# Kernel tuning notes

Hardware: AMD Instinct MI355X
Metric: run time of the kernel (lower is better)

The kernel has to match this reference:

```python
import jax, jax.numpy as jnp
import numpy as np

B, S, D, H, DK, CR = 4, 4096, 1024, 16, 64, 3


def setup_inputs() -> dict:
    rng = jax.random.key(0)
    ks = jax.random.split(rng, 13)
    sc = 1.0 / np.sqrt(D)
    u = lambda k, shape: jax.random.uniform(k, shape, jnp.float32, -sc, sc)
    return {
        "query": jax.random.normal(ks[0], (B, S, D), jnp.float32),
        "key": jax.random.normal(ks[1], (B, S, D), jnp.float32),
        "value": jax.random.normal(ks[2], (B, S, D), jnp.float32),
        "Wq": u(ks[3], (D, D)), "bq": u(ks[4], (D,)),
        "Wk": u(ks[5], (D, D)), "bk": u(ks[6], (D,)),
        "Wv": u(ks[7], (D, D)), "bv": u(ks[8], (D,)),
        "Wo": u(ks[9], (D, D)), "bo": u(ks[10], (D,)),
        "conv_w": u(ks[11], (D, D, CR)),  # Conv1d(D, D, kernel=CR, stride=CR)
        "conv_b": u(ks[12], (D,)),
    }


def _compress(x, w, b):
    # x: (B, L, D) -> strided conv over L -> (B, ceil-ish L/CR, D)
    y = jax.lax.conv_general_dilated(
        x.transpose(0, 2, 1), w, window_strides=(CR,), padding="VALID",
        dimension_numbers=("NCH", "OIH", "NCH"))
    return (y + b[None, :, None]).transpose(0, 2, 1)


def reference(query, key, value, Wq, bq, Wk, bk, Wv, bv, Wo, bo, conv_w, conv_b):
    # Source quirk: pad amount derived from d_model (last dim), applied to seq.
    pad = CR - D % CR  # = 2 here
    if pad < CR:
        key = jnp.pad(key, ((0, 0), (pad, 0), (0, 0)))
        value = jnp.pad(value, ((0, 0), (pad, 0), (0, 0)))
    key = _compress(key, conv_w, conv_b)
    value = _compress(value, conv_w, conv_b)

    def proj(x, W, bias):  # (B, L, D) -> (B, H, L, DK)
        return (x @ W.T + bias).reshape(x.shape[0], -1, H, DK).transpose(0, 2, 1, 3)

    q = proj(query, Wq, bq)
    k = proj(key, Wk, bk)
    v = proj(value, Wv, bv)

    scores = jnp.einsum("bhqd,bhkd->bhqk", q, k) / np.float32(np.sqrt(DK))
    attn = jax.nn.softmax(scores, axis=-1)  # dropout is identity at eval
    x = jnp.einsum("bhqk,bhkd->bhqd", attn, v)
    x = x.transpose(0, 2, 1, 3).reshape(query.shape[0], -1, H * DK)
    return x @ Wo.T + bo
```

## Files before the change

### kernel.cpp

```cpp
#include <hip/hip_runtime.h>


#define DM   1024
#define NH   16
#define DKH  64
#define BB   4
#define SQ   4096
#define LCC  1366
#define LCP  1408
#define SPAD 4098

#define QSC  0.18033688011f

typedef unsigned short u16;
using short8 = __attribute__((ext_vector_type(8))) short;
using f32x4  = __attribute__((ext_vector_type(4))) float;
using us4    = __attribute__((ext_vector_type(4))) unsigned short;
using us8    = __attribute__((ext_vector_type(8))) unsigned short;

__device__ __forceinline__ u16 f2bf(float f) {
    unsigned u = __float_as_uint(f);
    u += 0x7fffu + ((u >> 16) & 1u);
    return (u16)(u >> 16);
}

__device__ __forceinline__ void gl_lds16(const void* g, void* l) {
    __builtin_amdgcn_global_load_lds(
        (__attribute__((address_space(1))) unsigned int*)(uintptr_t)g,
        (__attribute__((address_space(3))) unsigned int*)l,
        16, 0, 0);
}

__global__ __launch_bounds__(256) void cast4_k(const float* __restrict__ in, u16* __restrict__ out,
                                               int n4, float scale) {
    int i = blockIdx.x * 256 + threadIdx.x;
    if (i >= n4) return;
    float4 v = ((const float4*)in)[i];
    us4 o;
    o[0] = f2bf(v.x * scale); o[1] = f2bf(v.y * scale);
    o[2] = f2bf(v.z * scale); o[3] = f2bf(v.w * scale);
    ((us4*)out)[i] = o;
}

__global__ __launch_bounds__(256) void cast_pad2_k(const float* __restrict__ in0, u16* __restrict__ out0,
                                                   const float* __restrict__ in1, u16* __restrict__ out1) {
    const float* in = blockIdx.z ? in1 : in0;
    u16* out        = blockIdx.z ? out1 : out0;
    int i = blockIdx.x * 256 + threadIdx.x;
    const int n4 = BB * SPAD * DM / 4;
    if (i >= n4) return;
    int e   = i * 4;
    int b   = e / (SPAD * DM);
    int rem = e - b * (SPAD * DM);
    int s   = rem >> 10;
    int d   = rem & (DM - 1);
    us4 o = {0, 0, 0, 0};
    if (s >= 2) {
        float4 v = *(const float4*)(in + (size_t)(b * SQ + (s - 2)) * DM + d);
        o[0] = f2bf(v.x); o[1] = f2bf(v.y); o[2] = f2bf(v.z); o[3] = f2bf(v.w);
    }
    ((us4*)out)[i] = o;
}

__global__ __launch_bounds__(256) void permcast_conv_k(const float* __restrict__ cw, u16* __restrict__ wc2) {
    int i = blockIdx.x * 256 + threadIdx.x;
    const int n4 = DM * DM * 3 / 4;
    if (i >= n4) return;
    int e   = i * 4;
    int o   = e / 3072;
    int rem = e - o * 3072;
    int r   = rem >> 10;
    int ii  = rem & 1023;
    us4 q;
    #pragma unroll
    for (int t = 0; t < 4; ++t) q[t] = f2bf(cw[(size_t)(o * DM + ii + t) * 3 + r]);
    ((us4*)wc2)[i] = q;
}

__global__ __launch_bounds__(256) void transpose_v_k(const u16* __restrict__ vp, u16* __restrict__ vt) {
    __shared__ u16 t[64 * 65];
    const int tid = threadIdx.x;
    const int j0 = blockIdx.x * 64;
    const int bh = blockIdx.y, b = bh >> 4, h = bh & 15;
    #pragma unroll
    for (int it = 0; it < 2; ++it) {
        int cc = tid + it * 256;
        int j = cc >> 3, d0 = (cc & 7) * 8;
        int jj = j0 + j;
        us8 v = {0, 0, 0, 0, 0, 0, 0, 0};
        if (jj < LCC) v = *(const us8*)(vp + (size_t)(b * LCC + jj) * DM + h * DKH + d0);
        #pragma unroll
        for (int q = 0; q < 8; ++q) t[(d0 + q) * 65 + j] = v[q];
    }
    __syncthreads();
    #pragma unroll
    for (int it = 0; it < 2; ++it) {
        int cc = tid + it * 256;
        int d = cc >> 3, q0 = (cc & 7) * 8;
        us8 v;
        #pragma unroll
        for (int q = 0; q < 8; ++q) {
            int cp = q0 + q;
            int ks = cp >> 5, qd = (cp >> 3) & 3, j = cp & 7;
            int k  = (ks + 2 * (j >> 2)) * 16 + qd * 4 + (j & 3);
            v[q] = t[d * 65 + k];
        }
        *(us8*)(vt + (size_t)(bh * DKH + d) * LCP + j0 + q0) = v;
    }
}

__global__ __launch_bounds__(256, 3) void gemm_mfma_k(
    const u16* __restrict__ A0, const u16* __restrict__ B0, const float* __restrict__ bias0, void* __restrict__ C0,
    const u16* __restrict__ A1, const u16* __restrict__ B1, const float* __restrict__ bias1, void* __restrict__ C1,
    int N, int K, int cf32, float bscale)
{
    const u16* A     = blockIdx.z ? A1 : A0;
    const u16* Bw    = blockIdx.z ? B1 : B0;
    const float* bias = blockIdx.z ? bias1 : bias0;
    void* C          = blockIdx.z ? C1 : C0;

    __shared__ u16 As[128 * 64];
    __shared__ u16 Bs[128 * 64];
    const int tid = threadIdx.x, wave = tid >> 6, lane = tid & 63;
    const int quad = lane >> 4, l15 = lane & 15;
    const int n0 = blockIdx.y * 128, o0 = blockIdx.x * 128;
    const int wm = (wave >> 1) * 64, wn = (wave & 1) * 64;

    f32x4 acc[4][4];
    #pragma unroll
    for (int a = 0; a < 4; ++a)
        #pragma unroll
        for (int b = 0; b < 4; ++b)
            #pragma unroll
            for (int r = 0; r < 4; ++r) acc[a][b][r] = 0.0f;

    const int srow = (lane >> 3);
    const int sc8  = (lane & 7);

    for (int kt = 0; kt < K; kt += 64) {
        #pragma unroll
        for (int i = 0; i < 4; ++i) {
            int is  = wave * 4 + i;
            int row = is * 8 + srow;
            int c   = sc8 ^ (row & 7);
            int ra  = n0 + row; if (ra > N - 1) ra = N - 1;
            gl_lds16(A  + (size_t)ra * K + kt + c * 8,          As + is * 512 + lane * 8);
            gl_lds16(Bw + (size_t)(o0 + row) * K + kt + c * 8,  Bs + is * 512 + lane * 8);
        }
        __syncthreads();
        #pragma unroll
        for (int ks = 0; ks < 2; ++ks) {
            short8 af[4], bf[4];
            #pragma unroll
            for (int mi = 0; mi < 4; ++mi) {
                int m = wm + mi * 16 + l15;
                int c = (ks * 4 + quad) ^ (m & 7);
                af[mi] = *(const short8*)(As + m * 64 + c * 8);
            }
            #pragma unroll
            for (int nj = 0; nj < 4; ++nj) {
                int n = wn + nj * 16 + l15;
                int c = (ks * 4 + quad) ^ (n & 7);
                bf[nj] = *(const short8*)(Bs + n * 64 + c * 8);
            }
            #pragma unroll
            for (int mi = 0; mi < 4; ++mi)
                #pragma unroll
                for (int nj = 0; nj < 4; ++nj)
                    acc[mi][nj] = __builtin_amdgcn_mfma_f32_16x16x32_bf16(af[mi], bf[nj], acc[mi][nj], 0, 0, 0);
        }
        __syncthreads();
    }
    #pragma unroll
    for (int mi = 0; mi < 4; ++mi) {
        #pragma unroll
        for (int r = 0; r < 4; ++r) {
            int n = n0 + wm + mi * 16 + quad * 4 + r;
            if (n < N) {
                #pragma unroll
                for (int nj = 0; nj < 4; ++nj) {
                    int o = o0 + wn + nj * 16 + l15;
                    float v = acc[mi][nj][r] + bias[o] * bscale;
                    if (cf32) ((float*)C)[(size_t)n * DM + o] = v;
                    else      ((u16*)C)[(size_t)n * DM + o] = f2bf(v);
                }
            }
        }
    }
}

__global__ __launch_bounds__(256, 3) void attn_mfma_k(
    const u16* __restrict__ qp, const u16* __restrict__ kp,
    const u16* __restrict__ vt, u16* __restrict__ xo)
{
    __shared__ u16 lds[4 * 4096];
    const int tid = threadIdx.x, wave = tid >> 6, lane = tid & 63;
    const int quad = lane >> 4, l15 = lane & 15;
    const int bh = blockIdx.y, b = bh >> 4, h = bh & 15;
    const int s0 = blockIdx.x * 128;
    const int wq = wave * 32;
    const int srow = lane >> 3, sc8 = lane & 7;

    #pragma unroll
    for (int i = 0; i < 4; ++i) {
        int is = wave * 4 + i;
        int row = is * 8 + srow;
        int c = sc8 ^ (row & 7);
        gl_lds16(qp + (size_t)(b * SQ + s0 + row) * DM + h * DKH + c * 8,
                 lds + is * 512 + lane * 8);
    }
    __syncthreads();
    short8 qfr[2][2];
    #pragma unroll
    for (int qg = 0; qg < 2; ++qg) {
        int m = wq + qg * 16 + l15;
        #pragma unroll
        for (int ks = 0; ks < 2; ++ks) {
            int c = (ks * 4 + quad) ^ (m & 7);
            qfr[qg][ks] = *(const short8*)(lds + m * 64 + c * 8);
        }
    }
    __syncthreads();

    f32x4 oacc[2][4];
    #pragma unroll
    for (int a = 0; a < 2; ++a)
        #pragma unroll
        for (int d = 0; d < 4; ++d)
            #pragma unroll
            for (int r = 0; r < 4; ++r) oacc[a][d][r] = 0.0f;
    float lsum[2] = {0.f, 0.f};

    #pragma unroll
    for (int i = 0; i < 2; ++i) {
        int is = wave * 2 + i;
        int row = is * 8 + srow;
        int c = sc8 ^ (row & 7);
        int j = row; if (j > LCC - 1) j = LCC - 1;
        gl_lds16(kp + (size_t)(b * LCC + j) * DM + h * DKH + c * 8, lds + is * 512 + lane * 8);
        gl_lds16(vt + (size_t)(bh * DKH + row) * LCP + c * 8,       lds + 4096 + is * 512 + lane * 8);
    }

    int cur = 0;
    for (int t = 0; t < 22; ++t) {
        const int j0 = t * 64;
        __syncthreads();
        if (t < 21) {
            int nj0 = j0 + 64;
            u16* base = lds + (cur ^ 1) * 8192;
            #pragma unroll
            for (int i = 0; i < 2; ++i) {
                int is = wave * 2 + i;
                int row = is * 8 + srow;
                int c = sc8 ^ (row & 7);
                int j = nj0 + row; if (j > LCC - 1) j = LCC - 1;
                gl_lds16(kp + (size_t)(b * LCC + j) * DM + h * DKH + c * 8, base + is * 512 + lane * 8);
                gl_lds16(vt + (size_t)(bh * DKH + row) * LCP + nj0 + c * 8, base + 4096 + is * 512 + lane * 8);
            }
        }
        const u16* Kb = lds + cur * 8192;
        const u16* Vb = Kb + 4096;

        f32x4 sc[2][4];
        #pragma unroll
        for (int a = 0; a < 2; ++a)
            #pragma unroll
            for (int n = 0; n < 4; ++n)
                #pragma unroll
                for (int r = 0; r < 4; ++r) sc[a][n][r] = 0.0f;
        __builtin_amdgcn_s_setprio(1);
        #pragma unroll
        for (int ks = 0; ks < 2; ++ks) {
            short8 kfr[4];
            #pragma unroll
            for (int nj = 0; nj < 4; ++nj) {
                int n = nj * 16 + l15;
                int c = (ks * 4 + quad) ^ (n & 7);
                kfr[nj] = *(const short8*)(Kb + n * 64 + c * 8);
            }
            #pragma unroll
            for (int qg = 0; qg < 2; ++qg)
                #pragma unroll
                for (int nj = 0; nj < 4; ++nj)
                    sc[qg][nj] = __builtin_amdgcn_mfma_f32_16x16x32_bf16(kfr[nj], qfr[qg][ks], sc[qg][nj], 0, 0, 0);
        }
        __builtin_amdgcn_s_setprio(0);

        const bool tail = (j0 + 64 > LCC);
        #pragma unroll
        for (int qg = 0; qg < 2; ++qg) {
            #pragma unroll
            for (int nj = 0; nj < 4; ++nj) {
                #pragma unroll
                for (int r = 0; r < 4; ++r) {
                    float p = __builtin_amdgcn_exp2f(sc[qg][nj][r]);
                    if (tail && (j0 + nj * 16 + quad * 4 + r) >= LCC) p = 0.0f;
                    sc[qg][nj][r] = p;
                    lsum[qg] += p;
                }
            }
        }
        short8 pa[2][2];
        #pragma unroll
        for (int qg = 0; qg < 2; ++qg) {
            #pragma unroll
            for (int ks = 0; ks < 2; ++ks) {
                unsigned w0, w1, w2, w3;
                asm("v_cvt_pk_bf16_f32 %0, %1, %2" : "=v"(w0) : "v"(sc[qg][ks][0]),     "v"(sc[qg][ks][1]));
                asm("v_cvt_pk_bf16_f32 %0, %1, %2" : "=v"(w1) : "v"(sc[qg][ks][2]),     "v"(sc[qg][ks][3]));
                asm("v_cvt_pk_bf16_f32 %0, %1, %2" : "=v"(w2) : "v"(sc[qg][ks + 2][0]), "v"(sc[qg][ks + 2][1]));
                asm("v_cvt_pk_bf16_f32 %0, %1, %2" : "=v"(w3) : "v"(sc[qg][ks + 2][2]), "v"(sc[qg][ks + 2][3]));
                union { unsigned u[4]; short8 s; } cv;
                cv.u[0] = w0; cv.u[1] = w1; cv.u[2] = w2; cv.u[3] = w3;
                pa[qg][ks] = cv.s;
            }
        }
        __builtin_amdgcn_s_setprio(1);
        #pragma unroll
        for (int ks = 0; ks < 2; ++ks) {
            short8 vfr[4];
            #pragma unroll
            for (int dj = 0; dj < 4; ++dj) {
                int d = dj * 16 + l15;
                int c = (ks * 4 + quad) ^ (d & 7);
                vfr[dj] = *(const short8*)(Vb + d * 64 + c * 8);
            }
            #pragma unroll
            for (int qg = 0; qg < 2; ++qg)
                #pragma unroll
                for (int dj = 0; dj < 4; ++dj)
                    oacc[qg][dj] = __builtin_amdgcn_mfma_f32_16x16x32_bf16(pa[qg][ks], vfr[dj], oacc[qg][dj], 0, 0, 0);
        }
        __builtin_amdgcn_s_setprio(0);
        cur ^= 1;
    }

    #pragma unroll
    for (int qg = 0; qg < 2; ++qg) {
        float v = lsum[qg];
        v += __shfl_xor(v, 16, 64);
        v += __shfl_xor(v, 32, 64);
        lsum[qg] = v;
    }
    #pragma unroll
    for (int qg = 0; qg < 2; ++qg) {
        #pragma unroll
        for (int r = 0; r < 4; ++r) {
            float tot = __shfl(lsum[qg], quad * 4 + r, 64);
            float inv = 1.0f / tot;
            int s = s0 + wq + qg * 16 + quad * 4 + r;
            #pragma unroll
            for (int dj = 0; dj < 4; ++dj)
                xo[(size_t)(b * SQ + s) * DM + h * DKH + dj * 16 + l15] = f2bf(oacc[qg][dj][r] * inv);
        }
    }
}

extern "C" void kernel_launch(void* const* d_in, const int* in_sizes, int n_in,
                              void* d_out, int out_size, void* d_ws, size_t ws_size,
                              hipStream_t stream)
{
    const float* query  = (const float*)d_in[0];
    const float* key    = (const float*)d_in[1];
    const float* value  = (const float*)d_in[2];
    const float* Wq     = (const float*)d_in[3];
    const float* bq     = (const float*)d_in[4];
    const float* Wk     = (const float*)d_in[5];
    const float* bk     = (const float*)d_in[6];
    const float* Wv     = (const float*)d_in[7];
    const float* bv     = (const float*)d_in[8];
    const float* Wo     = (const float*)d_in[9];
    const float* bo     = (const float*)d_in[10];
    const float* conv_w = (const float*)d_in[11];
    const float* conv_b = (const float*)d_in[12];
    float* out = (float*)d_out;

    u16* p = (u16*)d_ws;
    auto alloc = [&](size_t n) { u16* r = p; p += (n + 127) & ~(size_t)127; return r; };
    u16* qbf  = alloc((size_t)BB * SQ * DM);
    u16* kpad = alloc((size_t)BB * SPAD * DM);
    u16* vpad = alloc((size_t)BB * SPAD * DM);
    u16* wqb  = alloc((size_t)DM * DM);
    u16* wkb  = alloc((size_t)DM * DM);
    u16* wvb  = alloc((size_t)DM * DM);
    u16* wob  = alloc((size_t)DM * DM);
    u16* wc2b = alloc((size_t)DM * DM * 3);
    u16* kc   = alloc((size_t)BB * LCC * DM);
    u16* vc   = alloc((size_t)BB * LCC * DM);
    u16* kpj  = alloc((size_t)BB * LCC * DM);
    u16* vpj  = alloc((size_t)BB * LCC * DM);
    u16* qprj = alloc((size_t)BB * SQ * DM);
    u16* vtb  = alloc((size_t)BB * NH * DKH * LCP);
    u16* xo   = alloc((size_t)BB * SQ * DM);

    const int NC = BB * LCC;
    const int NS = BB * SQ;

    cast4_k<<<dim3(NS * DM / 4 / 256), 256, 0, stream>>>(query, qbf, NS * DM / 4, 1.0f);
    cast_pad2_k<<<dim3((BB * SPAD * DM / 4 + 255) / 256, 1, 2), 256, 0, stream>>>(key, kpad, value, vpad);
    cast4_k<<<dim3(DM * DM / 4 / 256), 256, 0, stream>>>(Wq, wqb, DM * DM / 4, QSC);
    cast4_k<<<dim3(DM * DM / 4 / 256), 256, 0, stream>>>(Wk, wkb, DM * DM / 4, 1.0f);
    cast4_k<<<dim3(DM * DM / 4 / 256), 256, 0, stream>>>(Wv, wvb, DM * DM / 4, 1.0f);
    cast4_k<<<dim3(DM * DM / 4 / 256), 256, 0, stream>>>(Wo, wob, DM * DM / 4, 1.0f);
    permcast_conv_k<<<dim3(DM * DM * 3 / 4 / 256), 256, 0, stream>>>(conv_w, wc2b);

    gemm_mfma_k<<<dim3(8, 43, 2), 256, 0, stream>>>(kpad, wc2b, conv_b, kc,
                                                    vpad, wc2b, conv_b, vc, NC, 3072, 0, 1.0f);

    gemm_mfma_k<<<dim3(8, 128, 1), 256, 0, stream>>>(qbf, wqb, bq, qprj,
                                                     qbf, wqb, bq, qprj, NS, DM, 0, QSC);
    gemm_mfma_k<<<dim3(8, 43, 2), 256, 0, stream>>>(kc, wkb, bk, kpj,
                                                    vc, wvb, bv, vpj, NC, DM, 0, 1.0f);

    transpose_v_k<<<dim3(22, BB * NH), 256, 0, stream>>>(vpj, vtb);

    attn_mfma_k<<<dim3(SQ / 128, BB * NH), 256, 0, stream>>>(qprj, kpj, vtb, xo);

    gemm_mfma_k<<<dim3(8, 128, 1), 256, 0, stream>>>(xo, wob, bo, out,
                                                     xo, wob, bo, out, NS, DM, 1, 1.0f);
}
```

Before: 603.2 us.

## Double-buffer GEMM LDS tiles, MFMA row sums in attention, batch weight casts

The GEMM kernel now double-buffers its A/B tiles in LDS. The next K tile is prefetched while MFMAs run on the current one, which leaves one barrier per iteration. To fit the doubled LDS, the occupancy hint drops from 3 to 2 blocks per CU. The attention kernel computes the softmax denominator with an extra MFMA against a vector of bf16 ones, replacing per-lane scalar adds and the cross-lane shuffle reduction, though this uses bf16-rounded probabilities for the sum. The four weight-cast launches are merged into a single grid-z launch.

```diff
diff --git a/kernel.cpp b/kernel.cpp
--- a/kernel.cpp
+++ b/kernel.cpp
@@ -35,6 +35,23 @@
                                                int n4, float scale) {
     int i = blockIdx.x * 256 + threadIdx.x;
     if (i >= n4) return;
+    float4 v = ((const float4*)in)[i];
+    us4 o;
+    o[0] = f2bf(v.x * scale); o[1] = f2bf(v.y * scale);
+    o[2] = f2bf(v.z * scale); o[3] = f2bf(v.w * scale);
+    ((us4*)out)[i] = o;
+}
+
+__global__ __launch_bounds__(256) void cast4w_k(
+    const float* __restrict__ w0, const float* __restrict__ w1,
+    const float* __restrict__ w2, const float* __restrict__ w3,
+    u16* __restrict__ o0, u16* __restrict__ o1, u16* __restrict__ o2, u16* __restrict__ o3,
+    float qsc) {
+    int z = blockIdx.z;
+    const float* in = (z == 0) ? w0 : (z == 1) ? w1 : (z == 2) ? w2 : w3;
+    u16* out        = (z == 0) ? o0 : (z == 1) ? o1 : (z == 2) ? o2 : o3;
+    float scale     = (z == 0) ? qsc : 1.0f;
+    int i = blockIdx.x * 256 + threadIdx.x;
     float4 v = ((const float4*)in)[i];
     us4 o;
     o[0] = f2bf(v.x * scale); o[1] = f2bf(v.y * scale);
@@ -109,22 +126,22 @@
     }
 }
 
-__global__ __launch_bounds__(256, 3) void gemm_mfma_k(
+__global__ __launch_bounds__(256, 2) void gemm_mfma_k(
     const u16* __restrict__ A0, const u16* __restrict__ B0, const float* __restrict__ bias0, void* __restrict__ C0,
     const u16* __restrict__ A1, const u16* __restrict__ B1, const float* __restrict__ bias1, void* __restrict__ C1,
     int N, int K, int cf32, float bscale)
 {
-    const u16* A     = blockIdx.z ? A1 : A0;
-    const u16* Bw    = blockIdx.z ? B1 : B0;
+    const u16* A      = blockIdx.z ? A1 : A0;
+    const u16* Bw     = blockIdx.z ? B1 : B0;
     const float* bias = blockIdx.z ? bias1 : bias0;
-    void* C          = blockIdx.z ? C1 : C0;
-
-    __shared__ u16 As[128 * 64];
-    __shared__ u16 Bs[128 * 64];
+    void* C           = blockIdx.z ? C1 : C0;
+
+    __shared__ u16 lds[2 * 16384];
     const int tid = threadIdx.x, wave = tid >> 6, lane = tid & 63;
     const int quad = lane >> 4, l15 = lane & 15;
     const int n0 = blockIdx.y * 128, o0 = blockIdx.x * 128;
     const int wm = (wave >> 1) * 64, wn = (wave & 1) * 64;
+    const int srow = (lane >> 3), sc8 = (lane & 7);
 
     f32x4 acc[4][4];
     #pragma unroll
@@ -134,20 +151,26 @@
             #pragma unroll
             for (int r = 0; r < 4; ++r) acc[a][b][r] = 0.0f;
 
-    const int srow = (lane >> 3);
-    const int sc8  = (lane & 7);
-
-    for (int kt = 0; kt < K; kt += 64) {
+    auto stage = [&](int kt, u16* base) {
         #pragma unroll
         for (int i = 0; i < 4; ++i) {
             int is  = wave * 4 + i;
             int row = is * 8 + srow;
             int c   = sc8 ^ (row & 7);
             int ra  = n0 + row; if (ra > N - 1) ra = N - 1;
-            gl_lds16(A  + (size_t)ra * K + kt + c * 8,          As + is * 512 + lane * 8);
-            gl_lds16(Bw + (size_t)(o0 + row) * K + kt + c * 8,  Bs + is * 512 + lane * 8);
-        }
+            gl_lds16(A  + (size_t)ra * K + kt + c * 8,          base + is * 512 + lane * 8);
+            gl_lds16(Bw + (size_t)(o0 + row) * K + kt + c * 8,  base + 8192 + is * 512 + lane * 8);
+        }
+    };
+
+    stage(0, lds);
+    int cur = 0;
+    const int nk = K >> 6;
+    for (int ki = 0; ki < nk; ++ki) {
         __syncthreads();
+        if (ki + 1 < nk) stage((ki + 1) << 6, lds + (cur ^ 1) * 16384);
+        const u16* As = lds + cur * 16384;
+        const u16* Bs = As + 8192;
         #pragma unroll
         for (int ks = 0; ks < 2; ++ks) {
             short8 af[4], bf[4];
@@ -169,7 +192,7 @@
                 for (int nj = 0; nj < 4; ++nj)
                     acc[mi][nj] = __builtin_amdgcn_mfma_f32_16x16x32_bf16(af[mi], bf[nj], acc[mi][nj], 0, 0, 0);
         }
-        __syncthreads();
+        cur ^= 1;
     }
     #pragma unroll
     for (int mi = 0; mi < 4; ++mi) {
@@ -222,14 +245,20 @@
     }
     __syncthreads();
 
-    f32x4 oacc[2][4];
-    #pragma unroll
-    for (int a = 0; a < 2; ++a)
+    f32x4 oacc[2][4], lacc[2];
+    #pragma unroll
+    for (int a = 0; a < 2; ++a) {
+        #pragma unroll
+        for (int r = 0; r < 4; ++r) lacc[a][r] = 0.0f;
         #pragma unroll
         for (int d = 0; d < 4; ++d)
             #pragma unroll
             for (int r = 0; r < 4; ++r) oacc[a][d][r] = 0.0f;
-    float lsum[2] = {0.f, 0.f};
+    }
+    union { unsigned u[4]; short8 s; } onesu;
+    #pragma unroll
+    for (int i = 0; i < 4; ++i) onesu.u[i] = 0x3f803f80u;
+    const short8 ones = onesu.s;
 
     #pragma unroll
     for (int i = 0; i < 2; ++i) {
@@ -296,7 +325,6 @@
                     float p = __builtin_amdgcn_exp2f(sc[qg][nj][r]);
                     if (tail && (j0 + nj * 16 + quad * 4 + r) >= LCC) p = 0.0f;
                     sc[qg][nj][r] = p;
-                    lsum[qg] += p;
                 }
             }
         }
@@ -326,10 +354,12 @@
                 vfr[dj] = *(const short8*)(Vb + d * 64 + c * 8);
             }
             #pragma unroll
-            for (int qg = 0; qg < 2; ++qg)
+            for (int qg = 0; qg < 2; ++qg) {
                 #pragma unroll
                 for (int dj = 0; dj < 4; ++dj)
                     oacc[qg][dj] = __builtin_amdgcn_mfma_f32_16x16x32_bf16(pa[qg][ks], vfr[dj], oacc[qg][dj], 0, 0, 0);
+                lacc[qg] = __builtin_amdgcn_mfma_f32_16x16x32_bf16(pa[qg][ks], ones, lacc[qg], 0, 0, 0);
+            }
         }
         __builtin_amdgcn_s_setprio(0);
         cur ^= 1;
@@ -337,17 +367,9 @@
 
     #pragma unroll
     for (int qg = 0; qg < 2; ++qg) {
-        float v = lsum[qg];
-        v += __shfl_xor(v, 16, 64);
-        v += __shfl_xor(v, 32, 64);
-        lsum[qg] = v;
-    }
-    #pragma unroll
-    for (int qg = 0; qg < 2; ++qg) {
         #pragma unroll
         for (int r = 0; r < 4; ++r) {
-            float tot = __shfl(lsum[qg], quad * 4 + r, 64);
-            float inv = 1.0f / tot;
+            float inv = 1.0f / lacc[qg][r];
             int s = s0 + wq + qg * 16 + quad * 4 + r;
             #pragma unroll
             for (int dj = 0; dj < 4; ++dj)
@@ -398,10 +420,7 @@
 
     cast4_k<<<dim3(NS * DM / 4 / 256), 256, 0, stream>>>(query, qbf, NS * DM / 4, 1.0f);
     cast_pad2_k<<<dim3((BB * SPAD * DM / 4 + 255) / 256, 1, 2), 256, 0, stream>>>(key, kpad, value, vpad);
-    cast4_k<<<dim3(DM * DM / 4 / 256), 256, 0, stream>>>(Wq, wqb, DM * DM / 4, QSC);
-    cast4_k<<<dim3(DM * DM / 4 / 256), 256, 0, stream>>>(Wk, wkb, DM * DM / 4, 1.0f);
-    cast4_k<<<dim3(DM * DM / 4 / 256), 256, 0, stream>>>(Wv, wvb, DM * DM / 4, 1.0f);
-    cast4_k<<<dim3(DM * DM / 4 / 256), 256, 0, stream>>>(Wo, wob, DM * DM / 4, 1.0f);
+    cast4w_k<<<dim3(DM * DM / 4 / 256, 1, 4), 256, 0, stream>>>(Wq, Wk, Wv, Wo, wqb, wkb, wvb, wob, QSC);
     permcast_conv_k<<<dim3(DM * DM * 3 / 4 / 256), 256, 0, stream>>>(conv_w, wc2b);
 
     gemm_mfma_k<<<dim3(8, 43, 2), 256, 0, stream>>>(kpad, wc2b, conv_b, kc,
```

New measurement: 644.5 us. +6.9%, slower.
